# Optimization experiments

Measured on AMD Instinct MI355X. Metric: run time of the kernel, lower is better.

Reference implementation:

```python
import jax, jax.numpy as jnp
import numpy as np

B, S, H, P = 8, 2048, 512, 16
K = H // 2

def setup_inputs() -> dict:
    key = jax.random.key(0)
    ks = jax.random.split(key, 6)
    sc_h = 1.0 / np.sqrt(H)
    sc_k = 1.0 / np.sqrt(K)
    return {
        "hidden_state": jax.random.normal(ks[0], (B, S, H), dtype=jnp.float32),
        "head_w": jax.random.normal(ks[1], (P, H), dtype=jnp.float32) * sc_h,
        "head_b": jnp.zeros((P,), dtype=jnp.float32),
        "embeds": jax.random.normal(ks[2], (P, H), dtype=jnp.float32),
        "w1": jax.random.normal(ks[3], (P, H, K), dtype=jnp.float32) * sc_h,
        "b1": jnp.zeros((P, K), dtype=jnp.float32),
        "w2": jax.random.normal(ks[4], (P, K, H), dtype=jnp.float32) * sc_k,
        "b2": jnp.zeros((P, H), dtype=jnp.float32),
    }

def reference(hidden_state, head_w, head_b, embeds, w1, b1, w2, b2):
    # Routing: pool over seq, linear head, softmax over programs -> (B, P)
    pooled = hidden_state.mean(axis=1)                      # (B, H)
    logits = jnp.einsum("bh,ph->bp", pooled, head_w) + head_b
    probs = jax.nn.softmax(logits, axis=-1)                  # (B, P)

    # Add program embedding per expert: (P, B, S, H)
    x = hidden_state[None, :, :, :] + embeds[:, None, None, :]
    # Expert MLP: Linear(H->K), exact GELU, Linear(K->H)
    mid = jax.nn.gelu(
        jnp.einsum("pbsh,phk->pbsk", x, w1) + b1[:, None, None, :],
        approximate=False,
    )
    adapted = jnp.einsum("pbsk,pkh->pbsh", mid, w2) + b2[:, None, None, :]
    # Weighted sum over programs with per-batch probs
    out = jnp.einsum("pbsh,bp->bsh", adapted, probs)         # (B, S, H)
    return out
```

## Files before the change

kernel.cpp:

```cpp
#include <hip/hip_runtime.h>
#include <hip/hip_bf16.h>
#include <stdint.h>

#define B_ 8
#define S_ 2048
#define H_ 512
#define P_ 16
#define K_ 256
#define M_TOT (B_*S_)
#define KCAT (P_*K_)

typedef short bf8v __attribute__((ext_vector_type(8)));
typedef float f4v  __attribute__((ext_vector_type(4)));

__device__ __align__(16) unsigned short g_hidden[M_TOT*H_];
__device__ __align__(16) unsigned short g_w1t[P_*K_*H_];
__device__ __align__(16) unsigned short g_w2cat[H_*KCAT];
__device__ __align__(16) unsigned short g_mid[(size_t)M_TOT*KCAT];
__device__ float g_bias1[P_*K_];

__device__ __forceinline__ unsigned short f2bf(float x){
  unsigned int u = __builtin_bit_cast(unsigned int, x);
  u += 0x7fffu + ((u >> 16) & 1u);
  return (unsigned short)(u >> 16);
}

__device__ __forceinline__ unsigned int pk2bf(float x, float y){
  return ((unsigned int)f2bf(y) << 16) | (unsigned int)f2bf(x);
}

__device__ __forceinline__ float gelu_prob(float x, float prob){
  float x2 = x*x;
  float t1 = 0.044715f*x;
  float u2 = fmaf(t1, x2, x);
  float e  = __expf(1.5957691216f*u2);
  float r  = __builtin_amdgcn_rcpf(e + 1.0f);
  float px = prob*x;
  return fmaf(-px, r, px);
}

__device__ __forceinline__ void gll16(const unsigned short* src, unsigned short* lds){
  __builtin_amdgcn_global_load_lds(
      (const __attribute__((address_space(1))) unsigned int*)src,
      (__attribute__((address_space(3))) unsigned int*)lds,
      16, 0, 0);
}

__device__ __forceinline__ void softmax16(const float* __restrict__ logits,
                                          const float* __restrict__ head_b,
                                          int b, float* lg, float* inv){
  float mx = -1e30f;
  #pragma unroll
  for (int pp=0; pp<P_; ++pp){
    lg[pp] = logits[b*P_+pp]*(1.0f/S_) + head_b[pp];
    mx = fmaxf(mx, lg[pp]);
  }
  float ssum = 0.0f;
  #pragma unroll
  for (int pp=0; pp<P_; ++pp){ lg[pp] = __expf(lg[pp]-mx); ssum += lg[pp]; }
  *inv = __builtin_amdgcn_rcpf(ssum);
}

__global__ void cvt_pool(const float* __restrict__ hs, float* __restrict__ logits,
                         const float* __restrict__ b1, const float* __restrict__ head_w){
  if (blockIdx.x < 16){
    g_bias1[blockIdx.x*256 + threadIdx.x] = b1[blockIdx.x*256 + threadIdx.x];
  }
  const int row0 = blockIdx.x * 64;
  const int b = row0 >> 11;
  const int tid = threadIdx.x;
  const int tx = tid & 127, ty = tid >> 7;
  const float4* src = (const float4*)(hs + (size_t)row0*H_) + tx;
  uint2* dst = (uint2*)g_hidden + (size_t)row0*(H_/4) + tx;
  float4 s = {0.f,0.f,0.f,0.f};
  for (int r = ty; r < 64; r += 2){
    float4 v = src[(size_t)r*128];
    s.x += v.x; s.y += v.y; s.z += v.z; s.w += v.w;
    uint2 o = { pk2bf(v.x, v.y), pk2bf(v.z, v.w) };
    dst[(size_t)r*128] = o;
  }
  __shared__ float4 red[256];
  red[tid] = s;
  __syncthreads();
  if (ty == 0){
    float4 a = red[tx], c = red[tx+128];
    float4 sf = { a.x+c.x, a.y+c.y, a.z+c.z, a.w+c.w };
    const float4* hw4 = (const float4*)head_w;
    float lp[P_];
    #pragma unroll
    for (int pp=0; pp<P_; ++pp){
      float4 hv = hw4[pp*128 + tx];
      lp[pp] = sf.x*hv.x + sf.y*hv.y + sf.z*hv.z + sf.w*hv.w;
    }
    #pragma unroll
    for (int off=32; off; off>>=1)
      #pragma unroll
      for (int pp=0; pp<P_; ++pp) lp[pp] += __shfl_down(lp[pp], off);
    if ((tid & 63) == 0){
      #pragma unroll
      for (int pp=0; pp<P_; ++pp) atomicAdd(&logits[b*P_+pp], lp[pp]);
    }
  }
}

__global__ void transpose_cvt_all(const float* __restrict__ w1,
                                  const float* __restrict__ w2,
                                  const float* __restrict__ embeds){
  const int tx = threadIdx.x & 31, ty = threadIdx.x >> 5;
  __shared__ float t[32][33];
  if (blockIdx.x < 2048){
    const int R = H_, C = K_;
    int p = blockIdx.x >> 7, rem = blockIdx.x & 127;
    int rt = rem >> 3, ct = rem & 7;
    const float* ip = w1 + (size_t)p*R*C + (size_t)(rt*32 + ty)*C + ct*32 + tx;
    #pragma unroll
    for (int k=0;k<4;++k) t[ty + 8*k][tx] = ip[(size_t)8*k*C];
    __syncthreads();
    unsigned short* op = g_w1t + (size_t)p*R*C + (size_t)(ct*32 + ty)*R + rt*32 + tx;
    #pragma unroll
    for (int k=0;k<4;++k) op[(size_t)8*k*R] = f2bf(t[tx][ty + 8*k]);
    if (ty == 0){
      float s = 0.0f;
      const float* ep = embeds + p*H_ + rt*32;
      #pragma unroll 8
      for (int hh=0; hh<32; ++hh) s = fmaf(ep[hh], t[hh][tx], s);
      atomicAdd(&g_bias1[p*K_ + ct*32 + tx], s);
    }
  } else {
    const int bid = blockIdx.x - 2048;
    const int R = K_, C = H_;
    int p = bid >> 7, rem = bid & 127;
    int rt = rem >> 4, ct = rem & 15;
    const float* ip = w2 + (size_t)p*R*C + (size_t)(rt*32 + ty)*C + ct*32 + tx;
    #pragma unroll
    for (int k=0;k<4;++k) t[ty + 8*k][tx] = ip[(size_t)8*k*C];
    __syncthreads();
    unsigned short* op = g_w2cat + (size_t)(ct*32 + ty)*KCAT + p*K_ + rt*32 + tx;
    #pragma unroll
    for (int k=0;k<4;++k) op[(size_t)8*k*KCAT] = f2bf(t[tx][ty + 8*k]);
  }
}


__device__ __forceinline__ void stage128(unsigned short* dst, const unsigned short* gsrc,
                                         int strideShorts, int koff, int tid){
  #pragma unroll
  for (int s = 0; s < 4; ++s){
    const int o   = (s*256 + tid)*8;
    const int row = o >> 6;
    const int ku  = (o & 63) >> 3;
    const int sku = ku ^ (row & 7);
    gll16(gsrc + (size_t)row*strideShorts + koff + sku*8, dst + o);
  }
}

__device__ __forceinline__ void kcompute(const unsigned short* Ab, const unsigned short* Bb,
    int rowA0, int rowB0, int l15, int lhi, f4v acc[4][4]){
  #pragma unroll
  for (int ksub=0; ksub<2; ++ksub){
    const int kb = ksub*64 + lhi*16;
    bf8v aF[4], bF[4];
    #pragma unroll
    for (int t=0; t<4; ++t){
      const int ra = rowA0 + t*16 + l15;
      aF[t] = *(const bf8v*)((const char*)Ab + ra*128 + (kb ^ ((ra&7)<<4)));
      const int rb = rowB0 + t*16 + l15;
      bF[t] = *(const bf8v*)((const char*)Bb + rb*128 + (kb ^ ((rb&7)<<4)));
    }
    __builtin_amdgcn_s_setprio(1);
    #pragma unroll
    for (int mt=0; mt<4; ++mt)
      #pragma unroll
      for (int nt=0; nt<4; ++nt)
        acc[mt][nt] = __builtin_amdgcn_mfma_f32_16x16x32_bf16(aF[mt], bF[nt], acc[mt][nt], 0,0,0);
    __builtin_amdgcn_s_setprio(0);
  }
}

__global__ __launch_bounds__(256, 4) void l1_kernel(const float* __restrict__ logits,
                                                   const float* __restrict__ head_b){
  __shared__ __align__(16) unsigned short lds[128*136];
  const int bid = blockIdx.x;
  const int xcd = bid & 7, i = bid >> 3;
  const int n0 = (xcd*4 + (i&3)) * 128;
  const int m0 = (i >> 2) * 128;
  const int p = n0 >> 8;
  const int b = m0 >> 11;
  const int tid = threadIdx.x, w = tid >> 6, lane = tid & 63;
  const int wm = w >> 1, wn = w & 1, l15 = lane & 15, lhi = lane >> 4;
  const unsigned short* gA = g_hidden + (size_t)m0 * H_;
  const unsigned short* gB = g_w1t + (size_t)n0 * H_;

  f4v acc[4][4];
  #pragma unroll
  for (int a=0;a<4;++a)
    #pragma unroll
    for (int c=0;c<4;++c) acc[a][c] = {0.f,0.f,0.f,0.f};

  for (int kt = 0; kt < 8; ++kt){
    stage128(lds,        gA, H_, kt*64, tid);
    stage128(lds + 8192, gB, H_, kt*64, tid);
    __syncthreads();
    kcompute(lds, lds + 8192, wm*64, wn*64, l15, lhi, acc);
    __syncthreads();
  }

  float lg[P_], inv;
  softmax16(logits, head_b, b, lg, &inv);
  const float prob = lg[p] * inv;

  #pragma unroll
  for (int nt=0; nt<4; ++nt){
    const int col = wn*64 + nt*16 + l15;
    const float bias = g_bias1[n0 + col];
    #pragma unroll
    for (int mt=0; mt<4; ++mt){
      const int r0 = wm*64 + mt*16 + lhi*4;
      unsigned int u01 = pk2bf(gelu_prob(acc[mt][nt][0] + bias, prob),
                               gelu_prob(acc[mt][nt][1] + bias, prob));
      unsigned int u23 = pk2bf(gelu_prob(acc[mt][nt][2] + bias, prob),
                               gelu_prob(acc[mt][nt][3] + bias, prob));
      lds[(r0+0)*136 + col] = (unsigned short)(u01 & 0xffffu);
      lds[(r0+1)*136 + col] = (unsigned short)(u01 >> 16);
      lds[(r0+2)*136 + col] = (unsigned short)(u23 & 0xffffu);
      lds[(r0+3)*136 + col] = (unsigned short)(u23 >> 16);
    }
  }
  __syncthreads();
  const int cc = tid & 15, rr = tid >> 4;
  #pragma unroll
  for (int pass=0; pass<8; ++pass){
    const int row = pass*16 + rr;
    bf8v vv = *(const bf8v*)&lds[row*136 + cc*8];
    *(bf8v*)&g_mid[(size_t)(m0+row)*KCAT + n0 + cc*8] = vv;
  }
}

__global__ __launch_bounds__(256, 2) void l2_kernel(float* __restrict__ out,
                                                   const float* __restrict__ b2,
                                                   const float* __restrict__ logits,
                                                   const float* __restrict__ head_b){
  __shared__ __align__(16) unsigned short lds[4*128*64];
  const int bid = blockIdx.x;
  const int xcd = bid & 7, i = bid >> 3;
  const int n0 = (i & 3) * 128;
  const int m0 = (xcd*16 + (i >> 2)) * 128;
  const int b = m0 >> 11;
  const int tid = threadIdx.x, w = tid >> 6, lane = tid & 63;
  const int wm = w >> 1, wn = w & 1, l15 = lane & 15, lhi = lane >> 4;
  const unsigned short* gA = g_mid + (size_t)m0 * KCAT;
  const unsigned short* gB = g_w2cat + (size_t)n0 * KCAT;

  f4v acc[4][4];
  #pragma unroll
  for (int a=0;a<4;++a)
    #pragma unroll
    for (int c=0;c<4;++c) acc[a][c] = {0.f,0.f,0.f,0.f};

  stage128(lds + 0,     gA, KCAT, 0, tid);
  stage128(lds + 16384, gB, KCAT, 0, tid);
  for (int kt = 0; kt < 64; ++kt){
    const int cur = kt & 1;
    if (kt < 63){
      stage128(lds + (cur ? 0 : 8192),         gA, KCAT, (kt+1)*64, tid);
      stage128(lds + 16384 + (cur ? 0 : 8192), gB, KCAT, (kt+1)*64, tid);
      asm volatile("s_waitcnt vmcnt(8)" ::: "memory");
    } else {
      asm volatile("s_waitcnt vmcnt(0)" ::: "memory");
    }
    __builtin_amdgcn_s_barrier();
    kcompute(lds + (cur ? 8192 : 0), lds + 16384 + (cur ? 8192 : 0),
             wm*64, wn*64, l15, lhi, acc);
    __builtin_amdgcn_s_barrier();
  }

  float lg[P_], inv;
  softmax16(logits, head_b, b, lg, &inv);

  #pragma unroll
  for (int nt=0; nt<4; ++nt){
    const int col = n0 + wn*64 + nt*16 + l15;
    float extra = 0.0f;
    #pragma unroll
    for (int pp=0; pp<P_; ++pp) extra = fmaf(lg[pp]*inv, b2[pp*H_ + col], extra);
    #pragma unroll
    for (int mt=0; mt<4; ++mt){
      #pragma unroll
      for (int j=0;j<4;++j){
        const int row = m0 + wm*64 + mt*16 + lhi*4 + j;
        out[(size_t)row*H_ + col] = acc[mt][nt][j] + extra;
      }
    }
  }
}

extern "C" void kernel_launch(void* const* d_in, const int* in_sizes, int n_in,
                              void* d_out, int out_size, void* d_ws, size_t ws_size,
                              hipStream_t stream){
  const float* hidden = (const float*)d_in[0];
  const float* head_w = (const float*)d_in[1];
  const float* head_b = (const float*)d_in[2];
  const float* embeds = (const float*)d_in[3];
  const float* w1     = (const float*)d_in[4];
  const float* b1     = (const float*)d_in[5];
  const float* w2     = (const float*)d_in[6];
  const float* b2     = (const float*)d_in[7];
  float* out = (float*)d_out;
  float* logits = (float*)d_ws;
  (void)in_sizes; (void)n_in; (void)out_size; (void)ws_size;

  (void)hipMemsetAsync(logits, 0, B_*P_*sizeof(float), stream);
  cvt_pool         <<<M_TOT/64, 256, 0, stream>>>(hidden, logits, b1, head_w);
  transpose_cvt_all<<<4096, 256, 0, stream>>>(w1, w2, embeds);
  l1_kernel        <<<4096, 256, 0, stream>>>(logits, head_b);
  l2_kernel        <<<512, 256, 0, stream>>>(out, b2, logits, head_b);
}
```

Measured before the change: 234.0 us.

## Merge prep kernels into one launch and double-buffer the L1 GEMM

The hidden-state conversion/pooling kernel and the weight transpose kernel become a single prepass launch. The embedding-bias accumulator moves into the zeroed workspace, and b1 is now added in the L1 epilogue. The L1 GEMM gets the same double-buffered LDS staging with vmcnt waits that L2 already uses, so the next tile's global loads overlap MFMA work. The larger LDS footprint lowers launch bounds from 4 to 2 blocks per CU, which may cut occupancy.

```diff
diff --git a/kernel.cpp b/kernel.cpp
--- a/kernel.cpp
+++ b/kernel.cpp
@@ -17,7 +17,7 @@
 __device__ __align__(16) unsigned short g_w1t[P_*K_*H_];
 __device__ __align__(16) unsigned short g_w2cat[H_*KCAT];
 __device__ __align__(16) unsigned short g_mid[(size_t)M_TOT*KCAT];
-__device__ float g_bias1[P_*K_];
+
 
 __device__ __forceinline__ unsigned short f2bf(float x){
   unsigned int u = __builtin_bit_cast(unsigned int, x);
@@ -61,54 +61,13 @@
   *inv = __builtin_amdgcn_rcpf(ssum);
 }
 
-__global__ void cvt_pool(const float* __restrict__ hs, float* __restrict__ logits,
-                         const float* __restrict__ b1, const float* __restrict__ head_w){
-  if (blockIdx.x < 16){
-    g_bias1[blockIdx.x*256 + threadIdx.x] = b1[blockIdx.x*256 + threadIdx.x];
-  }
-  const int row0 = blockIdx.x * 64;
-  const int b = row0 >> 11;
-  const int tid = threadIdx.x;
-  const int tx = tid & 127, ty = tid >> 7;
-  const float4* src = (const float4*)(hs + (size_t)row0*H_) + tx;
-  uint2* dst = (uint2*)g_hidden + (size_t)row0*(H_/4) + tx;
-  float4 s = {0.f,0.f,0.f,0.f};
-  for (int r = ty; r < 64; r += 2){
-    float4 v = src[(size_t)r*128];
-    s.x += v.x; s.y += v.y; s.z += v.z; s.w += v.w;
-    uint2 o = { pk2bf(v.x, v.y), pk2bf(v.z, v.w) };
-    dst[(size_t)r*128] = o;
-  }
-  __shared__ float4 red[256];
-  red[tid] = s;
-  __syncthreads();
-  if (ty == 0){
-    float4 a = red[tx], c = red[tx+128];
-    float4 sf = { a.x+c.x, a.y+c.y, a.z+c.z, a.w+c.w };
-    const float4* hw4 = (const float4*)head_w;
-    float lp[P_];
-    #pragma unroll
-    for (int pp=0; pp<P_; ++pp){
-      float4 hv = hw4[pp*128 + tx];
-      lp[pp] = sf.x*hv.x + sf.y*hv.y + sf.z*hv.z + sf.w*hv.w;
-    }
-    #pragma unroll
-    for (int off=32; off; off>>=1)
-      #pragma unroll
-      for (int pp=0; pp<P_; ++pp) lp[pp] += __shfl_down(lp[pp], off);
-    if ((tid & 63) == 0){
-      #pragma unroll
-      for (int pp=0; pp<P_; ++pp) atomicAdd(&logits[b*P_+pp], lp[pp]);
-    }
-  }
-}
-
-__global__ void transpose_cvt_all(const float* __restrict__ w1,
-                                  const float* __restrict__ w2,
-                                  const float* __restrict__ embeds){
-  const int tx = threadIdx.x & 31, ty = threadIdx.x >> 5;
+__global__ void prepass(const float* __restrict__ w1, const float* __restrict__ w2,
+                        const float* __restrict__ embeds,
+                        const float* __restrict__ hs, const float* __restrict__ head_w,
+                        float* __restrict__ ws){
   __shared__ float t[32][33];
   if (blockIdx.x < 2048){
+    const int tx = threadIdx.x & 31, ty = threadIdx.x >> 5;
     const int R = H_, C = K_;
     int p = blockIdx.x >> 7, rem = blockIdx.x & 127;
     int rt = rem >> 3, ct = rem & 7;
@@ -124,9 +83,10 @@
       const float* ep = embeds + p*H_ + rt*32;
       #pragma unroll 8
       for (int hh=0; hh<32; ++hh) s = fmaf(ep[hh], t[hh][tx], s);
-      atomicAdd(&g_bias1[p*K_ + ct*32 + tx], s);
-    }
-  } else {
+      atomicAdd(&ws[128 + p*K_ + ct*32 + tx], s);
+    }
+  } else if (blockIdx.x < 4096){
+    const int tx = threadIdx.x & 31, ty = threadIdx.x >> 5;
     const int bid = blockIdx.x - 2048;
     const int R = K_, C = H_;
     int p = bid >> 7, rem = bid & 127;
@@ -138,6 +98,42 @@
     unsigned short* op = g_w2cat + (size_t)(ct*32 + ty)*KCAT + p*K_ + rt*32 + tx;
     #pragma unroll
     for (int k=0;k<4;++k) op[(size_t)8*k*KCAT] = f2bf(t[tx][ty + 8*k]);
+  } else {
+    const int row0 = (blockIdx.x - 4096) * 64;
+    const int b = row0 >> 11;
+    const int tid = threadIdx.x;
+    const int tx = tid & 127, ty = tid >> 7;
+    const float4* src = (const float4*)(hs + (size_t)row0*H_) + tx;
+    uint2* dst = (uint2*)g_hidden + (size_t)row0*(H_/4) + tx;
+    float4 s = {0.f,0.f,0.f,0.f};
+    for (int r = ty; r < 64; r += 2){
+      float4 v = src[(size_t)r*128];
+      s.x += v.x; s.y += v.y; s.z += v.z; s.w += v.w;
+      uint2 o = { pk2bf(v.x, v.y), pk2bf(v.z, v.w) };
+      dst[(size_t)r*128] = o;
+    }
+    __shared__ float4 red[256];
+    red[tid] = s;
+    __syncthreads();
+    if (ty == 0){
+      float4 a = red[tx], c = red[tx+128];
+      float4 sf = { a.x+c.x, a.y+c.y, a.z+c.z, a.w+c.w };
+      const float4* hw4 = (const float4*)head_w;
+      float lp[P_];
+      #pragma unroll
+      for (int pp=0; pp<P_; ++pp){
+        float4 hv = hw4[pp*128 + tx];
+        lp[pp] = sf.x*hv.x + sf.y*hv.y + sf.z*hv.z + sf.w*hv.w;
+      }
+      #pragma unroll
+      for (int off=32; off; off>>=1)
+        #pragma unroll
+        for (int pp=0; pp<P_; ++pp) lp[pp] += __shfl_down(lp[pp], off);
+      if ((tid & 63) == 0){
+        #pragma unroll
+        for (int pp=0; pp<P_; ++pp) atomicAdd(&ws[b*P_+pp], lp[pp]);
+      }
+    }
   }
 }
 
@@ -177,9 +173,10 @@
   }
 }
 
-__global__ __launch_bounds__(256, 4) void l1_kernel(const float* __restrict__ logits,
-                                                   const float* __restrict__ head_b){
-  __shared__ __align__(16) unsigned short lds[128*136];
+__global__ __launch_bounds__(256, 2) void l1_kernel(const float* __restrict__ ws,
+                                                   const float* __restrict__ head_b,
+                                                   const float* __restrict__ b1){
+  __shared__ __align__(16) unsigned short lds[4*128*64];
   const int bid = blockIdx.x;
   const int xcd = bid & 7, i = bid >> 3;
   const int n0 = (xcd*4 + (i&3)) * 128;
@@ -197,22 +194,31 @@
     #pragma unroll
     for (int c=0;c<4;++c) acc[a][c] = {0.f,0.f,0.f,0.f};
 
+  stage128(lds + 0,     gA, H_, 0, tid);
+  stage128(lds + 16384, gB, H_, 0, tid);
   for (int kt = 0; kt < 8; ++kt){
-    stage128(lds,        gA, H_, kt*64, tid);
-    stage128(lds + 8192, gB, H_, kt*64, tid);
-    __syncthreads();
-    kcompute(lds, lds + 8192, wm*64, wn*64, l15, lhi, acc);
-    __syncthreads();
+    const int cur = kt & 1;
+    if (kt < 7){
+      stage128(lds + (cur ? 0 : 8192),         gA, H_, (kt+1)*64, tid);
+      stage128(lds + 16384 + (cur ? 0 : 8192), gB, H_, (kt+1)*64, tid);
+      asm volatile("s_waitcnt vmcnt(8)" ::: "memory");
+    } else {
+      asm volatile("s_waitcnt vmcnt(0)" ::: "memory");
+    }
+    __builtin_amdgcn_s_barrier();
+    kcompute(lds + (cur ? 8192 : 0), lds + 16384 + (cur ? 8192 : 0),
+             wm*64, wn*64, l15, lhi, acc);
+    __builtin_amdgcn_s_barrier();
   }
 
   float lg[P_], inv;
-  softmax16(logits, head_b, b, lg, &inv);
+  softmax16(ws, head_b, b, lg, &inv);
   const float prob = lg[p] * inv;
 
   #pragma unroll
   for (int nt=0; nt<4; ++nt){
     const int col = wn*64 + nt*16 + l15;
-    const float bias = g_bias1[n0 + col];
+    const float bias = ws[128 + n0 + col] + b1[n0 + col];
     #pragma unroll
     for (int mt=0; mt<4; ++mt){
       const int r0 = wm*64 + mt*16 + lhi*4;
@@ -238,7 +244,7 @@
 
 __global__ __launch_bounds__(256, 2) void l2_kernel(float* __restrict__ out,
                                                    const float* __restrict__ b2,
-                                                   const float* __restrict__ logits,
+                                                   const float* __restrict__ ws,
                                                    const float* __restrict__ head_b){
   __shared__ __align__(16) unsigned short lds[4*128*64];
   const int bid = blockIdx.x;
@@ -275,7 +281,7 @@
   }
 
   float lg[P_], inv;
-  softmax16(logits, head_b, b, lg, &inv);
+  softmax16(ws, head_b, b, lg, &inv);
 
   #pragma unroll
   for (int nt=0; nt<4; ++nt){
@@ -306,12 +312,11 @@
   const float* w2     = (const float*)d_in[6];
   const float* b2     = (const float*)d_in[7];
   float* out = (float*)d_out;
-  float* logits = (float*)d_ws;
+  float* ws  = (float*)d_ws;
   (void)in_sizes; (void)n_in; (void)out_size; (void)ws_size;
 
-  (void)hipMemsetAsync(logits, 0, B_*P_*sizeof(float), stream);
-  cvt_pool         <<<M_TOT/64, 256, 0, stream>>>(hidden, logits, b1, head_w);
-  transpose_cvt_all<<<4096, 256, 0, stream>>>(w1, w2, embeds);
-  l1_kernel        <<<4096, 256, 0, stream>>>(logits, head_b);
-  l2_kernel        <<<512, 256, 0, stream>>>(out, b2, logits, head_b);
-}
+  (void)hipMemsetAsync(ws, 0, (B_*P_ + P_*K_)*sizeof(float), stream);
+  prepass  <<<4096 + M_TOT/64, 256, 0, stream>>>(w1, w2, embeds, hidden, head_w, ws);
+  l1_kernel<<<4096, 256, 0, stream>>>(ws, head_b, b1);
+  l2_kernel<<<512, 256, 0, stream>>>(out, b2, ws, head_b);
+}
```

After: 236.0 us. No clear change (+0.9%).
